# Kernel optimization log

Hardware: AMD Instinct MI355X
Metric: run time of the kernel (lower is better)

The kernel has to match this reference:

```python
import jax, jax.numpy as jnp
import numpy as np

B, M, E, R = 4, 72, 24, 552          # docs, mentions/doc, entities/doc, pairs/doc
L, H, A = 1024, 1024, 16             # seq_len, hidden (LUKE-large), attn heads
EMB, BLK, OUT, NC = 768, 64, 768, 97 # embed_size, block_size, out_embed_size, num_class


def setup_inputs() -> dict:
    key = jax.random.key(0)
    ks = jax.random.split(key, 12)
    s = 0.02  # weight scale to keep tanh unsaturated
    return {
        "seq_lhs": jax.random.normal(ks[0], (B, L, H), jnp.float32),
        "ent_lhs": jax.random.normal(ks[1], (B, M, H), jnp.float32),
        "ent_to_seq_attn": jax.random.uniform(ks[2], (B, A, M, L), jnp.float32),
        "entity_id_labels": jax.random.randint(ks[3], (B, M), 0, E, jnp.int32),
        "hts": jax.random.randint(ks[4], (B, R, 2), 0, E, jnp.int32),
        "W_head": jax.random.normal(ks[5], (2 * H, EMB), jnp.float32) * s,
        "b_head": jnp.zeros((EMB,), jnp.float32),
        "W_tail": jax.random.normal(ks[6], (2 * H, EMB), jnp.float32) * s,
        "b_tail": jnp.zeros((EMB,), jnp.float32),
        "W_bil": jax.random.normal(ks[7], (EMB * BLK, OUT), jnp.float32) * s,
        "b_bil": jnp.zeros((OUT,), jnp.float32),
        "W_cls": jax.random.normal(ks[8], (OUT, NC), jnp.float32) * s,
        "b_cls": jnp.zeros((NC,), jnp.float32),
        "W_bin": jax.random.normal(ks[9], (OUT, 1), jnp.float32) * s,
        "b_bin": jnp.zeros((1,), jnp.float32),
    }


def _hrt_pool(seq_lhs, ent_lhs, ent_to_seq_attn, entity_id_labels, hts):
    # global segment id: doc_i * E + entity_label  -> [B*M]
    seg = (jnp.arange(B, dtype=entity_id_labels.dtype)[:, None] * E
           + entity_id_labels).reshape(-1)
    NSEG = B * E

    # --- entity embedding: logsumexp over mentions of each entity (0 if empty) ---
    x = ent_lhs.reshape(B * M, H)
    mx = jax.ops.segment_max(x, seg, num_segments=NSEG)          # -inf for empty
    mx_safe = jnp.where(jnp.isfinite(mx), mx, 0.0)
    ssum = jax.ops.segment_sum(jnp.exp(x - mx_safe[seg]), seg, num_segments=NSEG)
    cnt = jax.ops.segment_sum(jnp.ones((B * M,), x.dtype), seg, num_segments=NSEG)
    ent_emb = jnp.where(cnt[:, None] > 0, jnp.log(ssum) + mx_safe, 0.0)
    ent_emb = ent_emb.reshape(B, E, H)

    # --- entity-to-seq attention: mean over mentions (0 if empty) ---
    a = ent_to_seq_attn.transpose(0, 2, 1, 3).reshape(B * M, A, L)
    asum = jax.ops.segment_sum(a, seg, num_segments=NSEG)
    amean = jnp.where(cnt[:, None, None] > 0,
                      asum / jnp.maximum(cnt, 1.0)[:, None, None], 0.0)
    amean = amean.reshape(B, E, A, L)

    # --- gather head/tail per pair ---
    bidx = jnp.arange(B)[:, None]
    hs = ent_emb[bidx, hts[:, :, 0]]       # [B,R,H]
    ts = ent_emb[bidx, hts[:, :, 1]]
    ha = amean[bidx, hts[:, :, 0]]         # [B,R,A,L]
    ta = amean[bidx, hts[:, :, 1]]

    ht_attn = (ha * ta).mean(axis=2)       # [B,R,L] mean over heads
    ht_attn = ht_attn / (ht_attn.sum(axis=-1, keepdims=True) + 1e-5)
    rel = jnp.einsum('bld,brl->brd', seq_lhs, ht_attn)  # [B,R,H]
    return hs, ts, rel


def reference(seq_lhs, ent_lhs, ent_to_seq_attn, entity_id_labels, hts,
              W_head, b_head, W_tail, b_tail, W_bil, b_bil,
              W_cls, b_cls, W_bin, b_bin):
    hs, ts, rel = _hrt_pool(seq_lhs, ent_lhs, ent_to_seq_attn,
                            entity_id_labels, hts)
    N = B * R
    hs = jnp.tanh(jnp.concatenate([hs, rel], -1).reshape(N, 2 * H) @ W_head + b_head)
    ts = jnp.tanh(jnp.concatenate([ts, rel], -1).reshape(N, 2 * H) @ W_tail + b_tail)

    K = EMB // BLK
    b1 = hs.reshape(N, K, BLK)
    b2 = ts.reshape(N, K, BLK)
    bl = (b1[:, :, :, None] * b2[:, :, None, :]).reshape(N, EMB * BLK)
    embeds = bl @ W_bil + b_bil                    # [N, OUT]
    class_logits = embeds @ W_cls + b_cls          # [N, NC]
    binary_logits = embeds @ W_bin + b_bin         # [N, 1]
    return embeds, class_logits, binary_logits
```

## Files before the change

### kernel.cpp

```cpp
#include <hip/hip_runtime.h>
#include <hip/hip_bf16.h>
#include <math.h>
#include <stdint.h>

#define B_ 4
#define M_ 72
#define E_ 24
#define R_ 552
#define L_ 1024
#define H_ 1024
#define A_ 16
#define EMB_ 768
#define BLK_ 64
#define OUT_ 768
#define NC_ 97
#define N_ (B_*R_)
#define NPAD_ 2304
#define K2H_ (2*H_)
#define KB_ (EMB_/BLK_)
#define KTOT_ (EMB_*BLK_)
#define SLICE_ 1048576

typedef short s16x8 __attribute__((ext_vector_type(8)));
typedef float f32x4 __attribute__((ext_vector_type(4)));
typedef uint32_t u32x4 __attribute__((ext_vector_type(4)));

__device__ __forceinline__ uint32_t pkbf16(float lo, float hi) {
    uint32_t r;
    asm("v_cvt_pk_bf16_f32 %0, %1, %2" : "=v"(r) : "v"(lo), "v"(hi));
    return r;
}
__device__ __forceinline__ unsigned short f2bf(float f) {
    uint32_t u = __builtin_bit_cast(uint32_t, f);
    uint32_t r = (u + 0x7fffu + ((u >> 16) & 1u)) >> 16;
    return (unsigned short)r;
}
__device__ __forceinline__ float bff(unsigned short u) {
    return __builtin_bit_cast(float, (uint32_t)u << 16);
}
__device__ __forceinline__ void gload_lds16(const void* g, void* l) {
    __builtin_amdgcn_global_load_lds(
        (const __attribute__((address_space(1))) unsigned int*)g,
        (__attribute__((address_space(3))) unsigned int*)l, 16, 0, 0);
}

__global__ void k_pool(const float* __restrict__ ent_lhs,
                       const float* __restrict__ attn,
                       const int*   __restrict__ labels,
                       unsigned short* __restrict__ ent_bf,
                       unsigned short* __restrict__ amean_bf)
{
    int b = blockIdx.x / E_;
    int e = blockIdx.x % E_;
    __shared__ int mlist[M_];
    __shared__ int mcount;
    if (threadIdx.x == 0) {
        int c = 0;
        for (int m = 0; m < M_; ++m)
            if (labels[b*M_ + m] == e) mlist[c++] = m;
        mcount = c;
    }
    __syncthreads();
    int cnt = mcount;

    for (int h = threadIdx.x; h < H_; h += blockDim.x) {
        float out = 0.f;
        if (cnt > 0) {
            float mx = -INFINITY;
            for (int q = 0; q < cnt; ++q)
                mx = fmaxf(mx, ent_lhs[(size_t)(b*M_ + mlist[q])*H_ + h]);
            float s = 0.f;
            for (int q = 0; q < cnt; ++q)
                s += expf(ent_lhs[(size_t)(b*M_ + mlist[q])*H_ + h] - mx);
            out = logf(s) + mx;
        }
        ent_bf[(size_t)(b*E_ + e)*H_ + h] = f2bf(out);
    }

    float inv = (cnt > 0) ? (1.f / (float)cnt) : 0.f;
    for (int c4 = threadIdx.x; c4 < A_*(L_/4); c4 += blockDim.x) {
        int a = c4 / (L_/4), l4 = c4 % (L_/4);
        float sx = 0.f, sy = 0.f, sz = 0.f, sw = 0.f;
        for (int q = 0; q < cnt; ++q) {
            float4 v = *(const float4*)(attn + ((size_t)(b*A_ + a)*M_ + mlist[q])*L_ + l4*4);
            sx += v.x; sy += v.y; sz += v.z; sw += v.w;
        }
        ushort4 o;
        o.x = f2bf(sx*inv); o.y = f2bf(sy*inv); o.z = f2bf(sz*inv); o.w = f2bf(sw*inv);
        *(ushort4*)(amean_bf + ((size_t)(b*E_ + e)*A_ + a)*L_ + l4*4) = o;
    }
}

__global__ void k_htattn(const unsigned short* __restrict__ amean_bf,
                         const int* __restrict__ hts,
                         unsigned short* __restrict__ htw_bf)
{
    int br = blockIdx.x;
    int b  = br / R_;
    int hh = hts[br*2 + 0], tt = hts[br*2 + 1];
    const unsigned short* pa = amean_bf + (size_t)(b*E_ + hh)*A_*L_;
    const unsigned short* pb = amean_bf + (size_t)(b*E_ + tt)*A_*L_;

    int l0 = threadIdx.x * 4;
    float v[4] = {0.f, 0.f, 0.f, 0.f};
    for (int a = 0; a < A_; ++a) {
        ushort4 ua = *(const ushort4*)(pa + (size_t)a*L_ + l0);
        ushort4 ub = *(const ushort4*)(pb + (size_t)a*L_ + l0);
        v[0] += bff(ua.x)*bff(ub.x); v[1] += bff(ua.y)*bff(ub.y);
        v[2] += bff(ua.z)*bff(ub.z); v[3] += bff(ua.w)*bff(ub.w);
    }
    float part = (v[0]+v[1]+v[2]+v[3]) * 0.0625f;
    __shared__ float red[256];
    red[threadIdx.x] = part;
    __syncthreads();
    for (int st = 128; st > 0; st >>= 1) {
        if (threadIdx.x < st) red[threadIdx.x] += red[threadIdx.x + st];
        __syncthreads();
    }
    float norm = 0.0625f / (red[0] + 1e-5f);
    unsigned short* po = htw_bf + (size_t)br*L_ + l0;
    po[0] = f2bf(v[0]*norm); po[1] = f2bf(v[1]*norm);
    po[2] = f2bf(v[2]*norm); po[3] = f2bf(v[3]*norm);
}

__global__ void k_transcvt(const float* __restrict__ W, unsigned short* __restrict__ Wt,
                           int K, int O)
{
    const float* src = W + (size_t)blockIdx.z*K*O;
    unsigned short* dst = Wt + (size_t)blockIdx.z*K*O;
    __shared__ unsigned short t[64][72];
    int k0 = blockIdx.x * 64, o0 = blockIdx.y * 64;
    #pragma unroll
    for (int p = 0; p < 16; ++p) {
        int idx = p*256 + threadIdx.x;
        int r = idx >> 6, c = idx & 63;
        t[c][r] = f2bf(src[(size_t)(k0 + r)*O + o0 + c]);
    }
    __syncthreads();
    #pragma unroll
    for (int p = 0; p < 16; ++p) {
        int idx = p*256 + threadIdx.x;
        int r = idx >> 6, c = idx & 63;
        dst[(size_t)(o0 + r)*K + k0 + c] = t[r][c];
    }
}

__global__ void k_cvtW2(const float* __restrict__ W, unsigned short* __restrict__ W2)
{
    __shared__ unsigned short t[64][72];
    int k0 = blockIdx.x * 64, o0 = blockIdx.y * 64;
    #pragma unroll
    for (int p = 0; p < 16; ++p) {
        int idx = p*256 + threadIdx.x;
        int r = idx >> 6, c = idx & 63;
        t[c][r] = f2bf(W[(size_t)(k0 + r)*OUT_ + o0 + c]);
    }
    __syncthreads();
    int kb = k0 >> 12;
    int i  = (k0 >> 6) & 63;
    int ob = o0 >> 8;
    int wc = (o0 >> 7) & 1;
    int ofb = (o0 >> 4) & 7;
    unsigned short* base = W2 + (size_t)(kb*3 + ob)*SLICE_ + i*16384 + wc*8192;
    #pragma unroll
    for (int p = 0; p < 16; ++p) {
        int lin = p*256 + threadIdx.x;
        int e = lin & 7;
        int lane = (lin >> 3) & 63;
        int fl = lin >> 9;
        int jh = fl >> 2, ofl = fl & 3;
        int f = jh*8 + ofb + ofl;
        int j = (jh*4 + (lane >> 4))*8 + e;
        int o_local = ofl*16 + (lane & 15);
        base[f*512 + lane*8 + e] = t[o_local][j];
    }
}

__global__ void k_cvtWcat(const float* __restrict__ Wc, const float* __restrict__ Wbn,
                          unsigned short* __restrict__ WcatT)
{
    int idx = blockIdx.x*256 + threadIdx.x;
    if (idx < 256*768) {
        int o = idx / 768, k = idx % 768;
        float v = 0.f;
        if (o < NC_) v = Wc[(size_t)k*NC_ + o];
        else if (o == NC_) v = Wbn[k];
        WcatT[idx] = f2bf(v);
    }
}

__global__ __launch_bounds__(256, 2)
void k_rel_mfma(const unsigned short* __restrict__ htw,
                const unsigned short* __restrict__ seqT,
                unsigned short* __restrict__ rel_bf)
{
    int bid = blockIdx.x;
    int ot = bid & 7;
    int rest = bid >> 3;
    int mt = rest % 5;
    int b  = rest / 5;
    int m0 = mt*128, o0 = ot*128;
    int tid = threadIdx.x, lane = tid & 63, wid = tid >> 6;
    int wr = wid >> 1, wc = wid & 1;
    __shared__ __align__(16) unsigned short a_s[128*64];
    __shared__ __align__(16) unsigned short b_s[128*64];
    const unsigned short* Ab = htw + (size_t)b*R_*L_;
    const unsigned short* Bb = seqT + (size_t)b*H_*L_;

    u32x4 aR[4], bR[4];
    auto loadA = [&](int st) {
        #pragma unroll
        for (int q = 0; q < 4; ++q) {
            int slot = q*256 + tid;
            int r = slot >> 3, s = slot & 7;
            int ar = m0 + r; if (ar > R_-1) ar = R_-1;
            aR[q] = *(const u32x4*)(Ab + (size_t)ar*L_ + st*64 + s*8);
        }
    };
    auto loadB = [&](int st) {
        #pragma unroll
        for (int q = 0; q < 4; ++q) {
            int slot = q*256 + tid;
            int o = slot >> 3, s = slot & 7;
            bR[q] = *(const u32x4*)(Bb + (size_t)(o0+o)*L_ + st*64 + s*8);
        }
    };

    f32x4 acc[4][4];
    const f32x4 zz = {0.f,0.f,0.f,0.f};
    #pragma unroll
    for (int mf = 0; mf < 4; ++mf)
        #pragma unroll
        for (int of = 0; of < 4; ++of) acc[mf][of] = zz;

    loadA(0); loadB(0);
    for (int st = 0; st < 16; ++st) {
        __syncthreads();
        #pragma unroll
        for (int q = 0; q < 4; ++q) {
            int slot = q*256 + tid; int r = slot >> 3, s = slot & 7;
            *(u32x4*)((char*)a_s + r*128 + ((s ^ (r & 7)) << 4)) = aR[q];
        }
        #pragma unroll
        for (int q = 0; q < 4; ++q) {
            int slot = q*256 + tid; int o = slot >> 3, s = slot & 7;
            *(u32x4*)((char*)b_s + o*128 + ((s ^ (o & 7)) << 4)) = bR[q];
        }
        __syncthreads();
        if (st < 15) { loadA(st+1); loadB(st+1); }
        #pragma unroll
        for (int kh = 0; kh < 2; ++kh) {
            s16x8 af[4];
            #pragma unroll
            for (int mf = 0; mf < 4; ++mf) {
                int r = wr*64 + mf*16 + (lane & 15);
                int s = kh*4 + (lane >> 4);
                af[mf] = *(const s16x8*)((const char*)a_s + r*128 + ((s ^ (r & 7)) << 4));
            }
            #pragma unroll
            for (int of = 0; of < 4; ++of) {
                int ol = wc*64 + of*16 + (lane & 15);
                int s = kh*4 + (lane >> 4);
                s16x8 bfr = *(const s16x8*)((const char*)b_s + ol*128 + ((s ^ (ol & 7)) << 4));
                #pragma unroll
                for (int mf = 0; mf < 4; ++mf)
                    acc[mf][of] = __builtin_amdgcn_mfma_f32_16x16x32_bf16(
                        af[mf], bfr, acc[mf][of], 0, 0, 0);
            }
        }
    }
    #pragma unroll
    for (int mf = 0; mf < 4; ++mf)
        #pragma unroll
        for (int of = 0; of < 4; ++of) {
            int col = o0 + wc*64 + of*16 + (lane & 15);
            #pragma unroll
            for (int rr = 0; rr < 4; ++rr) {
                int row = m0 + wr*64 + mf*16 + (lane >> 4)*4 + rr;
                if (row < R_)
                    rel_bf[((size_t)b*R_ + row)*H_ + col] = f2bf(acc[mf][of][rr]);
            }
        }
}

__global__ void k_pinit(const float* __restrict__ b_head,
                        const float* __restrict__ b_tail,
                        float* __restrict__ pacc)
{
    int idx = blockIdx.x * 256 + threadIdx.x;
    if (idx < 2*NPAD_*OUT_) {
        const float* bb = (idx < NPAD_*OUT_) ? b_head : b_tail;
        pacc[idx] = bb[idx % OUT_];
    }
}

__global__ __launch_bounds__(256, 2)
void k_proj_mfma(const unsigned short* __restrict__ ent_bf,
                 const unsigned short* __restrict__ rel_bf,
                 const int* __restrict__ hts,
                 const unsigned short* __restrict__ Wph,
                 const unsigned short* __restrict__ Wpt,
                 float* __restrict__ pacc)
{
    int bid = blockIdx.x;
    int kq = bid & 3;
    int rest = bid >> 2;
    int ob = rest % 3;  rest /= 3;
    int mb = rest % 18;
    int which = rest / 18;
    int m0 = mb * 128, o0 = ob * 256;
    const unsigned short* Wp = which ? Wpt : Wph;
    float* out = pacc + (size_t)which*NPAD_*OUT_;
    int tid = threadIdx.x, lane = tid & 63, wid = tid >> 6;
    int wr = wid >> 1, wc = wid & 1;
    __shared__ __align__(16) unsigned short a_s[128*64];
    __shared__ __align__(16) unsigned short b_s[256*64];

    bool enthalf = (kq < 2);
    const unsigned short* abase[4];
    #pragma unroll
    for (int q = 0; q < 4; ++q) {
        int slot = q*256 + tid;
        int r = slot >> 3;
        int n = m0 + r;
        int nn = (n < N_) ? n : (N_ - 1);
        if (enthalf) {
            int bb = nn / R_;
            abase[q] = ent_bf + (size_t)(bb*E_ + hts[nn*2 + which])*H_ + kq*512;
        } else {
            abase[q] = rel_bf + (size_t)nn*H_ + (kq - 2)*512;
        }
    }
    u32x4 aR[4], bR[8];
    auto loadA = [&](int st) {
        #pragma unroll
        for (int q = 0; q < 4; ++q) {
            int s = (q*256 + tid) & 7;
            aR[q] = *(const u32x4*)(abase[q] + st*64 + s*8);
        }
    };
    auto loadB = [&](int st) {
        #pragma unroll
        for (int q = 0; q < 8; ++q) {
            int slot = q*256 + tid;
            int o = slot >> 3, s = slot & 7;
            bR[q] = *(const u32x4*)(Wp + (size_t)(o0+o)*K2H_ + kq*512 + st*64 + s*8);
        }
    };

    f32x4 acc[4][8];
    const f32x4 zz = {0.f,0.f,0.f,0.f};
    #pragma unroll
    for (int mf = 0; mf < 4; ++mf)
        #pragma unroll
        for (int of = 0; of < 8; ++of) acc[mf][of] = zz;

    loadA(0); loadB(0);
    for (int st = 0; st < 8; ++st) {
        __syncthreads();
        #pragma unroll
        for (int q = 0; q < 4; ++q) {
            int slot = q*256 + tid; int r = slot >> 3, s = slot & 7;
            *(u32x4*)((char*)a_s + r*128 + ((s ^ (r & 7)) << 4)) = aR[q];
        }
        #pragma unroll
        for (int q = 0; q < 8; ++q) {
            int slot = q*256 + tid; int o = slot >> 3, s = slot & 7;
            *(u32x4*)((char*)b_s + o*128 + ((s ^ (o & 7)) << 4)) = bR[q];
        }
        __syncthreads();
        if (st < 7) { loadA(st+1); loadB(st+1); }
        #pragma unroll
        for (int kh = 0; kh < 2; ++kh) {
            s16x8 af[4];
            #pragma unroll
            for (int mf = 0; mf < 4; ++mf) {
                int r = wr*64 + mf*16 + (lane & 15);
                int s = kh*4 + (lane >> 4);
                af[mf] = *(const s16x8*)((const char*)a_s + r*128 + ((s ^ (r & 7)) << 4));
            }
            #pragma unroll
            for (int of = 0; of < 8; ++of) {
                int ol = wc*128 + of*16 + (lane & 15);
                int s = kh*4 + (lane >> 4);
                s16x8 bfr = *(const s16x8*)((const char*)b_s + ol*128 + ((s ^ (ol & 7)) << 4));
                #pragma unroll
                for (int mf = 0; mf < 4; ++mf)
                    acc[mf][of] = __builtin_amdgcn_mfma_f32_16x16x32_bf16(
                        af[mf], bfr, acc[mf][of], 0, 0, 0);
            }
        }
    }
    #pragma unroll
    for (int mf = 0; mf < 4; ++mf)
        #pragma unroll
        for (int of = 0; of < 8; ++of) {
            int col = o0 + wc*128 + of*16 + (lane & 15);
            #pragma unroll
            for (int rr = 0; rr < 4; ++rr) {
                int row = m0 + wr*64 + mf*16 + (lane >> 4)*4 + rr;
                atomicAdd(&out[(size_t)row*OUT_ + col], acc[mf][of][rr]);
            }
        }
}

__global__ void k_tanhcvt(const float* __restrict__ pacc,
                          unsigned short* __restrict__ hsp,
                          unsigned short* __restrict__ tsp)
{
    int idx = blockIdx.x * 256 + threadIdx.x;
    if (idx < NPAD_*OUT_) {
        hsp[idx] = f2bf(tanhf(pacc[idx]));
        tsp[idx] = f2bf(tanhf(pacc[NPAD_*OUT_ + idx]));
    }
}

__global__ void k_bias_init(const float* __restrict__ bias, float* __restrict__ embeds)
{
    int idx = blockIdx.x * 256 + threadIdx.x;
    if (idx < N_*OUT_) embeds[idx] = bias[idx % OUT_];
}

__global__ __launch_bounds__(256, 2)
void k_bilinear_mfma(const unsigned short* __restrict__ hsp,
                     const unsigned short* __restrict__ tsp,
                     const unsigned short* __restrict__ W2,
                     float* __restrict__ embeds)
{
    int bid = blockIdx.x;
    int x = bid & 7, jj = bid >> 3;
    int g = jj / 18, mb = jj % 18;
    int sh = g*8 + x;
    int s = sh >> 1, ih = sh & 1;
    int kb = s / 3, ob = s % 3;
    int i0 = ih * 32;
    int m0 = mb * 128, o0 = ob * 256;
    int tid = threadIdx.x, lane = tid & 63, wid = tid >> 6;
    int wr = wid >> 1, wc = wid & 1;

    __shared__ __align__(16) char smem[81920];
    unsigned short* hs_s = (unsigned short*)smem;
    char* w0 = smem + 16384;
    char* w1 = smem + 49152;
    unsigned short* ts_s = (unsigned short*)w0;

    const unsigned short* Wsl = W2 + (size_t)s * SLICE_;

    u32x4 wReg[8];
    auto loadW = [&](int i) {
        const unsigned short* src = Wsl + (size_t)i*16384;
        #pragma unroll
        for (int q = 0; q < 8; ++q)
            wReg[q] = *(const u32x4*)(src + q*2048 + wid*512 + lane*8);
    };
    auto writeW = [&](char* dst) {
        #pragma unroll
        for (int q = 0; q < 8; ++q)
            *(u32x4*)(dst + q*4096 + wid*1024 + lane*16) = wReg[q];
    };

    #pragma unroll
    for (int q = 0; q < 4; ++q) {
        int slot = q*256 + tid;
        int r = slot >> 3, s7 = slot & 7;
        int gg = s7 ^ (r & 7);
        size_t srcoff = (size_t)(m0 + r)*EMB_ + kb*64 + (gg << 3);
        gload_lds16(hsp + srcoff, (char*)hs_s + (q*4096 + wid*1024));
        gload_lds16(tsp + srcoff, (char*)ts_s + (q*4096 + wid*1024));
    }
    loadW(i0);
    __syncthreads();

    float tsf[4][2][8];
    #pragma unroll
    for (int mf = 0; mf < 4; ++mf) {
        int r = wr*64 + mf*16 + (lane & 15);
        #pragma unroll
        for (int jh = 0; jh < 2; ++jh) {
            int s8 = jh*4 + (lane >> 4);
            u32x4 tv = *(const u32x4*)((const char*)ts_s + r*128 + ((s8 ^ (r & 7)) << 4));
            #pragma unroll
            for (int p = 0; p < 4; ++p) {
                tsf[mf][jh][2*p]   = __builtin_bit_cast(float, tv[p] << 16);
                tsf[mf][jh][2*p+1] = __builtin_bit_cast(float, tv[p] & 0xffff0000u);
            }
        }
    }
    __syncthreads();
    writeW(w0);
    loadW(i0 + 1);
    __syncthreads();

    f32x4 acc[4][8];
    const f32x4 zz = {0.f, 0.f, 0.f, 0.f};
    #pragma unroll
    for (int mf = 0; mf < 4; ++mf)
        #pragma unroll
        for (int of = 0; of < 8; ++of) acc[mf][of] = zz;

    for (int ii = 0; ii < 32; ++ii) {
        int i = i0 + ii;
        char* cur = (ii & 1) ? w1 : w0;
        char* nxt = (ii & 1) ? w0 : w1;

        if (ii < 31) writeW(nxt);
        if (ii < 30) loadW(i + 2);

        float hsf[4];
        #pragma unroll
        for (int mf = 0; mf < 4; ++mf) {
            int r = wr*64 + mf*16 + (lane & 15);
            int hb = r*128 + ((((i >> 3)) ^ (r & 7)) << 4) + (i & 7)*2;
            hsf[mf] = bff(*(const unsigned short*)((const char*)hs_s + hb));
        }
        const char* wq = cur + wc*16384;
        #pragma unroll
        for (int jh = 0; jh < 2; ++jh) {
            s16x8 afr[4];
            #pragma unroll
            for (int mf = 0; mf < 4; ++mf) {
                u32x4 a;
                #pragma unroll
                for (int p = 0; p < 4; ++p)
                    a[p] = pkbf16(hsf[mf]*tsf[mf][jh][2*p], hsf[mf]*tsf[mf][jh][2*p+1]);
                afr[mf] = __builtin_bit_cast(s16x8, a);
            }
            #pragma unroll
            for (int of = 0; of < 8; ++of) {
                s16x8 bfr = *(const s16x8*)(wq + (jh*8 + of)*1024 + lane*16);
                #pragma unroll
                for (int mf = 0; mf < 4; ++mf)
                    acc[mf][of] = __builtin_amdgcn_mfma_f32_16x16x32_bf16(
                        afr[mf], bfr, acc[mf][of], 0, 0, 0);
            }
        }
        __syncthreads();
    }

    #pragma unroll
    for (int mf = 0; mf < 4; ++mf) {
        #pragma unroll
        for (int of = 0; of < 8; ++of) {
            int col = o0 + wc*128 + of*16 + (lane & 15);
            #pragma unroll
            for (int rr = 0; rr < 4; ++rr) {
                int row = wr*64 + mf*16 + (lane >> 4)*4 + rr;
                int n = m0 + row;
                if (n < N_)
                    atomicAdd(&embeds[(size_t)n*OUT_ + col], acc[mf][of][rr]);
            }
        }
    }
}

__global__ void k_cvtemb(const float* __restrict__ embeds, unsigned short* __restrict__ emb_bf)
{
    int idx = blockIdx.x * 256 + threadIdx.x;
    if (idx < N_*OUT_) emb_bf[idx] = f2bf(embeds[idx]);
}

__global__ __launch_bounds__(256, 2)
void k_logits_mfma(const unsigned short* __restrict__ emb_bf,
                   const unsigned short* __restrict__ WcatT,
                   const float* __restrict__ bc, const float* __restrict__ bbn,
                   float* __restrict__ cls, float* __restrict__ bin)
{
    int m0 = blockIdx.x * 128;
    int tid = threadIdx.x, lane = tid & 63, wid = tid >> 6;
    int wr = wid >> 1, wc = wid & 1;
    __shared__ __align__(16) unsigned short a_s[128*64];
    __shared__ __align__(16) unsigned short b_s[256*64];

    u32x4 aR[4], bR[8];
    auto loadA = [&](int st) {
        #pragma unroll
        for (int q = 0; q < 4; ++q) {
            int slot = q*256 + tid;
            int r = slot >> 3, s = slot & 7;
            int ar = m0 + r; if (ar > N_-1) ar = N_-1;
            aR[q] = *(const u32x4*)(emb_bf + (size_t)ar*OUT_ + st*64 + s*8);
        }
    };
    auto loadB = [&](int st) {
        #pragma unroll
        for (int q = 0; q < 8; ++q) {
            int slot = q*256 + tid;
            int o = slot >> 3, s = slot & 7;
            bR[q] = *(const u32x4*)(WcatT + (size_t)o*OUT_ + st*64 + s*8);
        }
    };

    f32x4 acc[4][8];
    const f32x4 zz = {0.f,0.f,0.f,0.f};
    #pragma unroll
    for (int mf = 0; mf < 4; ++mf)
        #pragma unroll
        for (int of = 0; of < 8; ++of) acc[mf][of] = zz;

    loadA(0); loadB(0);
    for (int st = 0; st < 12; ++st) {
        __syncthreads();
        #pragma unroll
        for (int q = 0; q < 4; ++q) {
            int slot = q*256 + tid; int r = slot >> 3, s = slot & 7;
            *(u32x4*)((char*)a_s + r*128 + ((s ^ (r & 7)) << 4)) = aR[q];
        }
        #pragma unroll
        for (int q = 0; q < 8; ++q) {
            int slot = q*256 + tid; int o = slot >> 3, s = slot & 7;
            *(u32x4*)((char*)b_s + o*128 + ((s ^ (o & 7)) << 4)) = bR[q];
        }
        __syncthreads();
        if (st < 11) { loadA(st+1); loadB(st+1); }
        #pragma unroll
        for (int kh = 0; kh < 2; ++kh) {
            s16x8 af[4];
            #pragma unroll
            for (int mf = 0; mf < 4; ++mf) {
                int r = wr*64 + mf*16 + (lane & 15);
                int s = kh*4 + (lane >> 4);
                af[mf] = *(const s16x8*)((const char*)a_s + r*128 + ((s ^ (r & 7)) << 4));
            }
            #pragma unroll
            for (int of = 0; of < 8; ++of) {
                int ol = wc*128 + of*16 + (lane & 15);
                int s = kh*4 + (lane >> 4);
                s16x8 bfr = *(const s16x8*)((const char*)b_s + ol*128 + ((s ^ (ol & 7)) << 4));
                #pragma unroll
                for (int mf = 0; mf < 4; ++mf)
                    acc[mf][of] = __builtin_amdgcn_mfma_f32_16x16x32_bf16(
                        af[mf], bfr, acc[mf][of], 0, 0, 0);
            }
        }
    }
    #pragma unroll
    for (int mf = 0; mf < 4; ++mf)
        #pragma unroll
        for (int of = 0; of < 8; ++of) {
            int col = wc*128 + of*16 + (lane & 15);
            if (col <= NC_) {
                #pragma unroll
                for (int rr = 0; rr < 4; ++rr) {
                    int row = m0 + wr*64 + mf*16 + (lane >> 4)*4 + rr;
                    if (row < N_) {
                        float v = acc[mf][of][rr];
                        if (col < NC_) cls[(size_t)row*NC_ + col] = v + bc[col];
                        else           bin[row] = v + bbn[0];
                    }
                }
            }
        }
}

extern "C" void kernel_launch(void* const* d_in, const int* in_sizes, int n_in,
                              void* d_out, int out_size, void* d_ws, size_t ws_size,
                              hipStream_t stream) {
    const float* seq_lhs = (const float*)d_in[0];
    const float* ent_lhs = (const float*)d_in[1];
    const float* attn    = (const float*)d_in[2];
    const int*   labels  = (const int*)d_in[3];
    const int*   hts     = (const int*)d_in[4];
    const float* W_head  = (const float*)d_in[5];
    const float* b_head  = (const float*)d_in[6];
    const float* W_tail  = (const float*)d_in[7];
    const float* b_tail  = (const float*)d_in[8];
    const float* W_bil   = (const float*)d_in[9];
    const float* b_bil   = (const float*)d_in[10];
    const float* W_cls   = (const float*)d_in[11];
    const float* b_cls   = (const float*)d_in[12];
    const float* W_bin   = (const float*)d_in[13];
    const float* b_bin   = (const float*)d_in[14];

    float* out_embeds = (float*)d_out;
    float* out_cls    = out_embeds + (size_t)N_*OUT_;
    float* out_bin    = out_cls + (size_t)N_*NC_;

    float* ws = (float*)d_ws;
    size_t off = 0;
    unsigned short* ent_bf   = (unsigned short*)(ws + off); off += (size_t)B_*E_*H_/2;
    float* pacc = ws + off;
    unsigned short* amean_bf = (unsigned short*)(ws + off); off += (size_t)B_*E_*A_*L_/2;
    unsigned short* htw_bf   = (unsigned short*)(ws + off); off += (size_t)B_*R_*L_/2;
    unsigned short* seqT     = (unsigned short*)(ws + off); off += (size_t)B_*H_*L_/2;
    unsigned short* rel_bf   = (unsigned short*)(ws + off); off += (size_t)N_*H_/2;
    unsigned short* hsp      = (unsigned short*)(ws + off); off += (size_t)NPAD_*EMB_/2;
    unsigned short* tsp      = (unsigned short*)(ws + off); off += (size_t)NPAD_*EMB_/2;
    unsigned short* W2       = (unsigned short*)(ws + off); off += (size_t)OUT_*KTOT_/2;
    unsigned short* Wph      = (unsigned short*)(ws + off); off += (size_t)OUT_*K2H_/2;
    unsigned short* Wpt      = (unsigned short*)(ws + off); off += (size_t)OUT_*K2H_/2;
    unsigned short* WcatT    = (unsigned short*)(ws + off); off += (size_t)256*768/2;
    unsigned short* emb_bf   = (unsigned short*)(ws + off); off += (size_t)N_*OUT_/2;

    k_cvtW2<<<dim3(KTOT_/64, OUT_/64), 256, 0, stream>>>(W_bil, W2);
    k_transcvt<<<dim3(K2H_/64, OUT_/64, 1), 256, 0, stream>>>(W_head, Wph, K2H_, OUT_);
    k_transcvt<<<dim3(K2H_/64, OUT_/64, 1), 256, 0, stream>>>(W_tail, Wpt, K2H_, OUT_);
    k_transcvt<<<dim3(L_/64, H_/64, B_), 256, 0, stream>>>(seq_lhs, seqT, L_, H_);
    k_cvtWcat<<<(256*768)/256, 256, 0, stream>>>(W_cls, W_bin, WcatT);

    k_pool<<<B_*E_, 256, 0, stream>>>(ent_lhs, attn, labels, ent_bf, amean_bf);
    k_htattn<<<B_*R_, 256, 0, stream>>>(amean_bf, hts, htw_bf);
    k_rel_mfma<<<160, 256, 0, stream>>>(htw_bf, seqT, rel_bf);

    k_pinit<<<(2*NPAD_*OUT_ + 255)/256, 256, 0, stream>>>(b_head, b_tail, pacc);
    k_proj_mfma<<<2*18*3*4, 256, 0, stream>>>(ent_bf, rel_bf, hts, Wph, Wpt, pacc);
    k_tanhcvt<<<(NPAD_*OUT_ + 255)/256, 256, 0, stream>>>(pacc, hsp, tsp);

    k_bias_init<<<(N_*OUT_ + 255)/256, 256, 0, stream>>>(b_bil, out_embeds);
    k_bilinear_mfma<<<1296, 256, 0, stream>>>(hsp, tsp, W2, out_embeds);

    k_cvtemb<<<(N_*OUT_ + 255)/256, 256, 0, stream>>>(out_embeds, emb_bf);
    k_logits_mfma<<<18, 256, 0, stream>>>(emb_bf, WcatT, b_cls, b_bin,
                                          out_cls, out_bin);
}
```

Before: 519.6 us.

## Load bilinear weight fragments directly from global into registers, drop LDS staging

The bilinear MFMA kernel now tiles the output into 128-column slices covering the full 64-element inner block, instead of 256-column slices split over two halves of the inner loop. The weight repack kernel is changed to match this layout. Each wave now loads its B fragments straight from global memory into registers with a double-buffered prefetch, removing the LDS weight staging and the per-iteration block barrier. The trade-off is that weights are no longer shared across waves through LDS, so the two row-waves each read them from global or cache. The accumulator tile per wave also shrinks, which should lower register pressure.

Result: faster. 475.2 us (-8.5%).

```diff
diff --git a/kernel.cpp b/kernel.cpp
--- a/kernel.cpp
+++ b/kernel.cpp
@@ -19,7 +19,7 @@
 #define K2H_ (2*H_)
 #define KB_ (EMB_/BLK_)
 #define KTOT_ (EMB_*BLK_)
-#define SLICE_ 1048576
+#define SLICE2_ 524288
 
 typedef short s16x8 __attribute__((ext_vector_type(8)));
 typedef float f32x4 __attribute__((ext_vector_type(4)));
@@ -158,18 +158,16 @@
     __syncthreads();
     int kb = k0 >> 12;
     int i  = (k0 >> 6) & 63;
-    int ob = o0 >> 8;
-    int wc = (o0 >> 7) & 1;
-    int ofb = (o0 >> 4) & 7;
-    unsigned short* base = W2 + (size_t)(kb*3 + ob)*SLICE_ + i*16384 + wc*8192;
+    int ob = o0 >> 7;
+    int wc = (o0 >> 6) & 1;
+    unsigned short* base = W2 + (size_t)(kb*6 + ob)*SLICE2_ + i*8192 + wc*4096;
     #pragma unroll
     for (int p = 0; p < 16; ++p) {
         int lin = p*256 + threadIdx.x;
         int e = lin & 7;
         int lane = (lin >> 3) & 63;
-        int fl = lin >> 9;
-        int jh = fl >> 2, ofl = fl & 3;
-        int f = jh*8 + ofb + ofl;
+        int f = lin >> 9;
+        int jh = f >> 2, ofl = f & 3;
         int j = (jh*4 + (lane >> 4))*8 + e;
         int o_local = ofl*16 + (lane & 15);
         base[f*512 + lane*8 + e] = t[o_local][j];
@@ -428,36 +426,16 @@
                      float* __restrict__ embeds)
 {
     int bid = blockIdx.x;
-    int x = bid & 7, jj = bid >> 3;
-    int g = jj / 18, mb = jj % 18;
-    int sh = g*8 + x;
-    int s = sh >> 1, ih = sh & 1;
-    int kb = s / 3, ob = s % 3;
-    int i0 = ih * 32;
-    int m0 = mb * 128, o0 = ob * 256;
+    int x = bid & 7, rest = bid >> 3;
+    int g = rest / 18, mb = rest % 18;
+    int s = g*8 + x;
+    int kb = s / 6, ob = s % 6;
+    int m0 = mb * 128;
     int tid = threadIdx.x, lane = tid & 63, wid = tid >> 6;
     int wr = wid >> 1, wc = wid & 1;
 
-    __shared__ __align__(16) char smem[81920];
-    unsigned short* hs_s = (unsigned short*)smem;
-    char* w0 = smem + 16384;
-    char* w1 = smem + 49152;
-    unsigned short* ts_s = (unsigned short*)w0;
-
-    const unsigned short* Wsl = W2 + (size_t)s * SLICE_;
-
-    u32x4 wReg[8];
-    auto loadW = [&](int i) {
-        const unsigned short* src = Wsl + (size_t)i*16384;
-        #pragma unroll
-        for (int q = 0; q < 8; ++q)
-            wReg[q] = *(const u32x4*)(src + q*2048 + wid*512 + lane*8);
-    };
-    auto writeW = [&](char* dst) {
-        #pragma unroll
-        for (int q = 0; q < 8; ++q)
-            *(u32x4*)(dst + q*4096 + wid*1024 + lane*16) = wReg[q];
-    };
+    __shared__ __align__(16) unsigned short hs_s[128*64];
+    __shared__ __align__(16) unsigned short ts_s[128*64];
 
     #pragma unroll
     for (int q = 0; q < 4; ++q) {
@@ -468,7 +446,6 @@
         gload_lds16(hsp + srcoff, (char*)hs_s + (q*4096 + wid*1024));
         gload_lds16(tsp + srcoff, (char*)ts_s + (q*4096 + wid*1024));
     }
-    loadW(i0);
     __syncthreads();
 
     float tsf[4][2][8];
@@ -486,26 +463,24 @@
             }
         }
     }
-    __syncthreads();
-    writeW(w0);
-    loadW(i0 + 1);
-    __syncthreads();
-
-    f32x4 acc[4][8];
+
+    const unsigned short* Wsl = W2 + (size_t)s * SLICE2_ + wc*4096 + lane*8;
+
+    f32x4 acc[4][4];
     const f32x4 zz = {0.f, 0.f, 0.f, 0.f};
     #pragma unroll
     for (int mf = 0; mf < 4; ++mf)
         #pragma unroll
-        for (int of = 0; of < 8; ++of) acc[mf][of] = zz;
-
-    for (int ii = 0; ii < 32; ++ii) {
-        int i = i0 + ii;
-        char* cur = (ii & 1) ? w1 : w0;
-        char* nxt = (ii & 1) ? w0 : w1;
-
-        if (ii < 31) writeW(nxt);
-        if (ii < 30) loadW(i + 2);
-
+        for (int of = 0; of < 4; ++of) acc[mf][of] = zz;
+
+    u32x4 bA[8], bB[8];
+    auto loadB = [&](int i, u32x4 (&buf)[8]) {
+        const unsigned short* src = Wsl + (size_t)i*8192;
+        #pragma unroll
+        for (int f = 0; f < 8; ++f)
+            buf[f] = *(const u32x4*)(src + f*512);
+    };
+    auto compute = [&](int i, u32x4 (&buf)[8]) {
         float hsf[4];
         #pragma unroll
         for (int mf = 0; mf < 4; ++mf) {
@@ -513,7 +488,6 @@
             int hb = r*128 + ((((i >> 3)) ^ (r & 7)) << 4) + (i & 7)*2;
             hsf[mf] = bff(*(const unsigned short*)((const char*)hs_s + hb));
         }
-        const char* wq = cur + wc*16384;
         #pragma unroll
         for (int jh = 0; jh < 2; ++jh) {
             s16x8 afr[4];
@@ -526,22 +500,29 @@
                 afr[mf] = __builtin_bit_cast(s16x8, a);
             }
             #pragma unroll
-            for (int of = 0; of < 8; ++of) {
-                s16x8 bfr = *(const s16x8*)(wq + (jh*8 + of)*1024 + lane*16);
+            for (int of = 0; of < 4; ++of) {
+                s16x8 bfr = __builtin_bit_cast(s16x8, buf[jh*4 + of]);
                 #pragma unroll
                 for (int mf = 0; mf < 4; ++mf)
                     acc[mf][of] = __builtin_amdgcn_mfma_f32_16x16x32_bf16(
                         afr[mf], bfr, acc[mf][of], 0, 0, 0);
             }
         }
-        __syncthreads();
+    };
+
+    loadB(0, bA);
+    for (int i2 = 0; i2 < 32; ++i2) {
+        loadB(2*i2 + 1, bB);
+        compute(2*i2, bA);
+        if (i2 < 31) loadB(2*i2 + 2, bA);
+        compute(2*i2 + 1, bB);
     }
 
     #pragma unroll
     for (int mf = 0; mf < 4; ++mf) {
         #pragma unroll
-        for (int of = 0; of < 8; ++of) {
-            int col = o0 + wc*128 + of*16 + (lane & 15);
+        for (int of = 0; of < 4; ++of) {
+            int col = ob*128 + wc*64 + of*16 + (lane & 15);
             #pragma unroll
             for (int rr = 0; rr < 4; ++rr) {
                 int row = wr*64 + mf*16 + (lane >> 4)*4 + rr;
```
